# Performance work log

Measured on AMD Instinct MI355X. Metric: run time of the kernel, lower is better.

## Reference

```python
import jax, jax.numpy as jnp
import numpy as np

# Regularized layout for the per-batch masked attention:
#   batch_size B=8, each batch has NF=2048 'fill' points followed by NK=4096 'keep' points.
B, NF, NK = 8, 2048, 4096
C_IN, C_KQ, C_OUT = 256, 64, 256


def setup_inputs() -> dict:
    key = jax.random.key(0)
    ks = jax.random.split(key, 7)
    N = B * (NF + NK)
    features = jax.random.normal(ks[0], (N, C_IN), dtype=jnp.float32)
    # keep flag: 0 for fill points, 1 for keep points, per batch (fill-first layout)
    flag = jnp.tile(jnp.concatenate([jnp.zeros(NF, jnp.int32), jnp.ones(NK, jnp.int32)]), B)
    s = 1.0 / np.sqrt(C_IN)
    Wq = jax.random.normal(ks[1], (C_KQ, C_IN), jnp.float32) * s
    bq = jnp.zeros((C_KQ,), jnp.float32)
    Wk = jax.random.normal(ks[2], (C_KQ, C_IN), jnp.float32) * s
    bk = jnp.zeros((C_KQ,), jnp.float32)
    Wv = jax.random.normal(ks[3], (C_OUT, C_IN), jnp.float32) * s
    bv = jnp.zeros((C_OUT,), jnp.float32)
    return {"features": features, "keep_flag": flag,
            "Wq": Wq, "bq": bq, "Wk": Wk, "bk": bk, "Wv": Wv, "bv": bv}


def reference(features, keep_flag, Wq, bq, Wk, bk, Wv, bv):
    # features: [N, C_IN]; keep_flag encodes the fill/keep split, which in this
    # regular layout is: first NF rows of each batch are fill, remaining NK are keep.
    del keep_flag  # structure is encoded in the layout (fill-first per batch)
    f = features.reshape(B, NF + NK, C_IN)
    fill = f[:, :NF]             # [B, NF, C_IN]
    keep = f[:, NF:]             # [B, NK, C_IN]
    q = fill @ Wq.T + bq         # [B, NF, C_KQ]
    k = keep @ Wk.T + bk         # [B, NK, C_KQ]
    v = keep @ Wv.T + bv         # [B, NK, C_OUT]
    ratio = np.sqrt(C_KQ).astype(np.float32)
    scores = jnp.einsum('bfd,bkd->bfk', q, k) / ratio   # [B, NF, NK]
    attn = jax.nn.softmax(scores, axis=-1)
    out_fill = jnp.einsum('bfk,bkc->bfc', attn, v)      # [B, NF, C_OUT]
    # keep rows pass through unchanged (only fill rows are overwritten)
    out = jnp.concatenate([out_fill, keep], axis=1)
    return out.reshape(B * (NF + NK), C_OUT)
```

## Files before the change

kernel.cpp:

```cpp
#include <hip/hip_runtime.h>
#include <hip/hip_bf16.h>

#define BATCHES 8
#define NFILL 2048
#define NKEEP 4096
#define SEQLEN 6144
#define CIN 256
#define CKQ 64
#define COUT 256

#define KSC 0.18033688011112042f
#define KOFF -11.541560327111707f

typedef __bf16 bf16_t;
typedef float f32x4 __attribute__((ext_vector_type(4)));
typedef bf16_t bf16x8 __attribute__((ext_vector_type(8)));

__device__ inline void cvt8_store(bf16_t* dst, float4 a, float4 b) {
  bf16x8 v;
  v[0] = (bf16_t)a.x; v[1] = (bf16_t)a.y; v[2] = (bf16_t)a.z; v[3] = (bf16_t)a.w;
  v[4] = (bf16_t)b.x; v[5] = (bf16_t)b.y; v[6] = (bf16_t)b.z; v[7] = (bf16_t)b.w;
  *(bf16x8*)dst = v;
}

__global__ __launch_bounds__(256) void gemm_qk(
    const float* __restrict__ feat, const float* __restrict__ Wq,
    const float* __restrict__ bq, const float* __restrict__ Wk,
    const float* __restrict__ bk, bf16_t* __restrict__ Qw,
    bf16_t* __restrict__ Kw) {
  __shared__ bf16_t Xs[64][72];
  __shared__ bf16_t Ws[64][72];

  const int QBLOCKS = BATCHES * NFILL / 64;
  const bool isK = blockIdx.x >= QBLOCKS;
  const int mb = isK ? blockIdx.x - QBLOCKS : blockIdx.x;
  const float* W = isK ? Wk : Wq;
  const float* bias = isK ? bk : bq;
  bf16_t* outp = isK ? Kw : Qw;
  const int rpb_shift = isK ? 12 : 11;
  const int row_off = isK ? NFILL : 0;

  const int t = threadIdx.x;
  const int lane = t & 63;
  const int wv = t >> 6;
  const int l16 = lane & 15;
  const int quad = lane >> 4;

  const int lr = t >> 2;
  const int koff = (t & 3) << 4;
  const int mrow = mb * 64 + lr;
  const int batch = mrow >> rpb_shift;
  const int ridx = mrow & ((1 << rpb_shift) - 1);
  const float* xptr = feat + ((long)(batch * SEQLEN + row_off + ridx)) * CIN + koff;
  const float* wptr = W + ((long)lr) * CIN + koff;

  f32x4 acc[4];
#pragma unroll
  for (int nb = 0; nb < 4; nb++) acc[nb] = f32x4{0.f, 0.f, 0.f, 0.f};

  for (int k0 = 0; k0 < CIN; k0 += 64) {
    float4 x0 = *(const float4*)(xptr + k0);
    float4 x1 = *(const float4*)(xptr + k0 + 4);
    float4 x2 = *(const float4*)(xptr + k0 + 8);
    float4 x3 = *(const float4*)(xptr + k0 + 12);
    float4 w0 = *(const float4*)(wptr + k0);
    float4 w1 = *(const float4*)(wptr + k0 + 4);
    float4 w2 = *(const float4*)(wptr + k0 + 8);
    float4 w3 = *(const float4*)(wptr + k0 + 12);
    __syncthreads();
    cvt8_store(&Xs[lr][koff], x0, x1);
    cvt8_store(&Xs[lr][koff + 8], x2, x3);
    cvt8_store(&Ws[lr][koff], w0, w1);
    cvt8_store(&Ws[lr][koff + 8], w2, w3);
    __syncthreads();
#pragma unroll
    for (int ks = 0; ks < 2; ks++) {
      bf16x8 afrag = *(const bf16x8*)&Xs[wv * 16 + l16][ks * 32 + quad * 8];
#pragma unroll
      for (int nb = 0; nb < 4; nb++) {
        bf16x8 bfrag = *(const bf16x8*)&Ws[nb * 16 + l16][ks * 32 + quad * 8];
        acc[nb] = __builtin_amdgcn_mfma_f32_16x16x32_bf16(afrag, bfrag, acc[nb], 0, 0, 0);
      }
    }
  }

#pragma unroll
  for (int nb = 0; nb < 4; nb++) {
    const int n = nb * 16 + l16;
    const float bb = bias[n];
#pragma unroll
    for (int r = 0; r < 4; r++) {
      const int m = mb * 64 + wv * 16 + quad * 4 + r;
      outp[(long)m * CKQ + n] = (bf16_t)(acc[nb][r] + bb);
    }
  }
}

__global__ __launch_bounds__(256) void gemm_v(
    const float* __restrict__ feat, const float* __restrict__ Wv,
    const float* __restrict__ bv, bf16_t* __restrict__ Vw,
    float* __restrict__ outp) {
  __shared__ bf16_t Xs[64][264];
  __shared__ bf16_t Ws[64][72];
  __shared__ float Cs[64][68];

  const int mb = blockIdx.x;
  const int t = threadIdx.x;
  const int lane = t & 63;
  const int wv = t >> 6;
  const int l16 = lane & 15;
  const int quad = lane >> 4;

  const int lr = t >> 2;
  const int koff = (t & 3) << 4;

  const int grow = mb * 64 + lr;
  const int batch = grow >> 12;
  const int ridx = grow & 4095;
  const float* xptr = feat + ((long)(batch * SEQLEN + NFILL + ridx)) * CIN;
  float4* orow = (float4*)(outp + ((long)(batch * SEQLEN + NFILL + ridx)) * COUT);

#pragma unroll
  for (int j = 0; j < 4; j++) {
    const int c = koff + j * 64;
    float4 x0 = *(const float4*)(xptr + c);
    float4 x1 = *(const float4*)(xptr + c + 4);
    float4 x2 = *(const float4*)(xptr + c + 8);
    float4 x3 = *(const float4*)(xptr + c + 12);
    cvt8_store(&Xs[lr][c], x0, x1);
    cvt8_store(&Xs[lr][c + 8], x2, x3);
    orow[(c >> 2) + 0] = x0;
    orow[(c >> 2) + 1] = x1;
    orow[(c >> 2) + 2] = x2;
    orow[(c >> 2) + 3] = x3;
  }
  __syncthreads();

  const int vb = (mb * 64) >> 12;
  const int key0base = (mb * 64) & 4095;

  for (int nt = 0; nt < 4; nt++) {
    const int n0 = nt * 64;
    f32x4 acc[4];
#pragma unroll
    for (int nb = 0; nb < 4; nb++) acc[nb] = f32x4{0.f, 0.f, 0.f, 0.f};

    for (int k0 = 0; k0 < CIN; k0 += 64) {
      const float* wptr = Wv + ((long)(n0 + lr)) * CIN + k0 + koff;
      float4 w0 = *(const float4*)(wptr);
      float4 w1 = *(const float4*)(wptr + 4);
      float4 w2 = *(const float4*)(wptr + 8);
      float4 w3 = *(const float4*)(wptr + 12);
      __syncthreads();
      cvt8_store(&Ws[lr][koff], w0, w1);
      cvt8_store(&Ws[lr][koff + 8], w2, w3);
      __syncthreads();
#pragma unroll
      for (int ks = 0; ks < 2; ks++) {
        bf16x8 afrag = *(const bf16x8*)&Xs[wv * 16 + l16][k0 + ks * 32 + quad * 8];
#pragma unroll
        for (int nb = 0; nb < 4; nb++) {
          bf16x8 bfrag = *(const bf16x8*)&Ws[nb * 16 + l16][ks * 32 + quad * 8];
          acc[nb] = __builtin_amdgcn_mfma_f32_16x16x32_bf16(afrag, bfrag, acc[nb], 0, 0, 0);
        }
      }
    }

    __syncthreads();
#pragma unroll
    for (int nb = 0; nb < 4; nb++) {
      const float bb = bv[n0 + nb * 16 + l16];
#pragma unroll
      for (int r = 0; r < 4; r++)
        Cs[wv * 16 + quad * 4 + r][nb * 16 + l16] = acc[nb][r] + bb;
    }
    __syncthreads();
    const int c = t >> 2;
    const int seg = t & 3;
    bf16_t tmp[16];
#pragma unroll
    for (int i = 0; i < 16; i++) tmp[i] = (bf16_t)Cs[seg * 16 + i][c];
    bf16_t* dst = Vw + ((long)(vb * COUT + n0 + c)) * NKEEP + key0base + seg * 16;
    *(uint4*)dst = *(uint4*)tmp;
    *(uint4*)(dst + 8) = *(uint4*)(tmp + 8);
  }
}

__global__ __launch_bounds__(256) void attn_kernel(
    const bf16_t* __restrict__ Q, const bf16_t* __restrict__ K,
    const bf16_t* __restrict__ Vt, float* __restrict__ outp) {
  __shared__ bf16_t Ks[2][64][72];
  __shared__ bf16_t Ps[64][72];
  __shared__ float Lsh[64];

  const int qt = blockIdx.x;
  const int b = blockIdx.y;
  const int t = threadIdx.x;
  const int lane = t & 63;
  const int wv = t >> 6;
  const int l16 = lane & 15;
  const int quad = lane >> 4;

  const int krow = t >> 2;
  const int kcol = (t & 3) << 4;

  const bf16_t* kbase = K + (long)b * NKEEP * CKQ;
  const int c0 = wv * 64;
  const bf16_t* vlane =
      Vt + ((long)(b * COUT + c0 + l16)) * NKEEP + quad * 8;

  bf16x8 qfrag[2];
  {
    const bf16_t* qrow = Q + ((long)(b * NFILL + qt * 64 + wv * 16 + l16)) * CKQ;
#pragma unroll
    for (int ks = 0; ks < 2; ks++)
      qfrag[ks] = *(const bf16x8*)(qrow + ks * 32 + quad * 8);
  }

  f32x4 oacc[4][4];
#pragma unroll
  for (int m = 0; m < 4; m++)
#pragma unroll
    for (int ct = 0; ct < 4; ct++) oacc[m][ct] = f32x4{0.f, 0.f, 0.f, 0.f};
  float rsum[4] = {0.f, 0.f, 0.f, 0.f};

  uint4 kreg0, kreg1;
  bf16x8 vA[8], vB[8];

  {
    const bf16_t* ksrc = kbase + (long)krow * CKQ + kcol;
    uint4 k0 = *(const uint4*)ksrc;
    uint4 k1 = *(const uint4*)(ksrc + 8);
#pragma unroll
    for (int ct = 0; ct < 4; ct++)
#pragma unroll
      for (int ks = 0; ks < 2; ks++)
        vA[ct * 2 + ks] = *(const bf16x8*)(vlane + (long)ct * 16 * NKEEP + ks * 32);
    *(uint4*)&Ks[0][krow][kcol] = k0;
    *(uint4*)&Ks[0][krow][kcol + 8] = k1;
  }

#define ATTN_TILE(BUF, VCUR, VNEXT, TV)                                         \
  {                                                                             \
    __syncthreads(); \
    const int tn = ((TV) + 1 < 64) ? (TV) + 1 : 63;                             \
    {                                                                           \
      const bf16_t* ksrc = kbase + ((long)(tn * 64 + krow)) * CKQ + kcol;       \
      kreg0 = *(const uint4*)ksrc;                                              \
      kreg1 = *(const uint4*)(ksrc + 8);                                        \
      const bf16_t* vsrc = vlane + (long)tn * 64;                               \
      _Pragma("unroll") for (int ct = 0; ct < 4; ct++)                          \
          _Pragma("unroll") for (int ks = 0; ks < 2; ks++)                      \
              VNEXT[ct * 2 + ks] =                                              \
          *(const bf16x8*)(vsrc + (long)ct * 16 * NKEEP + ks * 32);             \
    }                                                                           \
    f32x4 sacc[4];                                                              \
    _Pragma("unroll") for (int nb = 0; nb < 4; nb++)                            \
        sacc[nb] = f32x4{0.f, 0.f, 0.f, 0.f};                                   \
    _Pragma("unroll") for (int ks = 0; ks < 2; ks++) {                          \
      _Pragma("unroll") for (int nb = 0; nb < 4; nb++) {                        \
        bf16x8 kfrag = *(const bf16x8*)&Ks[BUF][nb * 16 + l16][ks * 32 + quad * 8]; \
        sacc[nb] = __builtin_amdgcn_mfma_f32_16x16x32_bf16(qfrag[ks], kfrag,    \
                                                           sacc[nb], 0, 0, 0); \
      }                                                                         \
    }                                                                           \
    _Pragma("unroll") for (int nb = 0; nb < 4; nb++) {                          \
      _Pragma("unroll") for (int r = 0; r < 4; r++) {                           \
        const float p = __builtin_exp2f(fmaf(sacc[nb][r], KSC, KOFF));          \
        rsum[r] += p;                                                           \
        Ps[wv * 16 + quad * 4 + r][nb * 16 + l16] = (bf16_t)p;                  \
      }                                                                         \
    }                                                                           \
    asm volatile("s_waitcnt lgkmcnt(0)\n\ts_barrier" ::: "memory");      \
    _Pragma("unroll") for (int ks = 0; ks < 2; ks++) {                          \
      _Pragma("unroll") for (int m = 0; m < 4; m++) {                           \
        bf16x8 pfrag = *(const bf16x8*)&Ps[m * 16 + l16][ks * 32 + quad * 8];   \
        _Pragma("unroll") for (int ct = 0; ct < 4; ct++)                        \
            oacc[m][ct] = __builtin_amdgcn_mfma_f32_16x16x32_bf16(              \
                pfrag, VCUR[ct * 2 + ks], oacc[m][ct], 0, 0, 0);                \
      }                                                                         \
    }                                                                           \
    *(uint4*)&Ks[BUF ^ 1][krow][kcol] = kreg0;                                  \
    *(uint4*)&Ks[BUF ^ 1][krow][kcol + 8] = kreg1;                              \
  }

#pragma unroll 1
  for (int tv = 0; tv < 64; tv += 2) {
    ATTN_TILE(0, vA, vB, tv)
    ATTN_TILE(1, vB, vA, tv + 1)
  }
#undef ATTN_TILE

#pragma unroll
  for (int off = 1; off < 16; off <<= 1)
#pragma unroll
    for (int r = 0; r < 4; r++) rsum[r] += __shfl_xor(rsum[r], off, 64);
  if (l16 == 0) {
#pragma unroll
    for (int r = 0; r < 4; r++) Lsh[wv * 16 + quad * 4 + r] = rsum[r];
  }
  __syncthreads();

  float rl[4][4];
#pragma unroll
  for (int m = 0; m < 4; m++)
#pragma unroll
    for (int r = 0; r < 4; r++) rl[m][r] = 1.0f / Lsh[m * 16 + quad * 4 + r];

  const long obase = ((long)(b * SEQLEN + qt * 64)) * COUT + c0;
#pragma unroll
  for (int m = 0; m < 4; m++)
#pragma unroll
    for (int ct = 0; ct < 4; ct++)
#pragma unroll
      for (int r = 0; r < 4; r++)
        outp[obase + (long)(m * 16 + quad * 4 + r) * COUT + ct * 16 + l16] =
            oacc[m][ct][r] * rl[m][r];
}

extern "C" void kernel_launch(void* const* d_in, const int* in_sizes, int n_in,
                              void* d_out, int out_size, void* d_ws, size_t ws_size,
                              hipStream_t stream) {
  const float* feat = (const float*)d_in[0];
  const float* Wq = (const float*)d_in[2];
  const float* bq = (const float*)d_in[3];
  const float* Wk = (const float*)d_in[4];
  const float* bk = (const float*)d_in[5];
  const float* Wv = (const float*)d_in[6];
  const float* bv = (const float*)d_in[7];
  float* outp = (float*)d_out;

  bf16_t* Qw = (bf16_t*)d_ws;
  bf16_t* Kw = Qw + (size_t)BATCHES * NFILL * CKQ;
  bf16_t* Vw = Kw + (size_t)BATCHES * NKEEP * CKQ;

  gemm_qk<<<dim3(768), 256, 0, stream>>>(feat, Wq, bq, Wk, bk, Qw, Kw);
  gemm_v<<<dim3(512), 256, 0, stream>>>(feat, Wv, bv, Vw, outp);
  attn_kernel<<<dim3(NFILL / 64, BATCHES), 256, 0, stream>>>(Qw, Kw, Vw, outp);
}
```

Before: 216.0 us.

## Load K fragments directly to registers and double-buffer P in LDS

```diff
diff --git a/kernel.cpp b/kernel.cpp
--- a/kernel.cpp
+++ b/kernel.cpp
@@ -15,6 +15,7 @@
 typedef __bf16 bf16_t;
 typedef float f32x4 __attribute__((ext_vector_type(4)));
 typedef bf16_t bf16x8 __attribute__((ext_vector_type(8)));
+typedef bf16_t bf16x4 __attribute__((ext_vector_type(4)));
 
 __device__ inline void cvt8_store(bf16_t* dst, float4 a, float4 b) {
   bf16x8 v;
@@ -189,8 +190,7 @@
 __global__ __launch_bounds__(256) void attn_kernel(
     const bf16_t* __restrict__ Q, const bf16_t* __restrict__ K,
     const bf16_t* __restrict__ Vt, float* __restrict__ outp) {
-  __shared__ bf16_t Ks[2][64][72];
-  __shared__ bf16_t Ps[64][72];
+  __shared__ bf16_t Ps[2][64][72];
   __shared__ float Lsh[64];
 
   const int qt = blockIdx.x;
@@ -201,10 +201,8 @@
   const int l16 = lane & 15;
   const int quad = lane >> 4;
 
-  const int krow = t >> 2;
-  const int kcol = (t & 3) << 4;
-
-  const bf16_t* kbase = K + (long)b * NKEEP * CKQ;
+  const bf16_t* klane =
+      K + ((long)(b * NKEEP + l16)) * CKQ + quad * 8;
   const int c0 = wv * 64;
   const bf16_t* vlane =
       Vt + ((long)(b * COUT + c0 + l16)) * NKEEP + quad * 8;
@@ -222,83 +220,79 @@
   for (int m = 0; m < 4; m++)
 #pragma unroll
     for (int ct = 0; ct < 4; ct++) oacc[m][ct] = f32x4{0.f, 0.f, 0.f, 0.f};
-  float rsum[4] = {0.f, 0.f, 0.f, 0.f};
-
-  uint4 kreg0, kreg1;
-  bf16x8 vA[8], vB[8];
+  float rsum = 0.f;
+
+  bf16x8 kA[8], kB[8], vA[8], vB[8];
 
   {
-    const bf16_t* ksrc = kbase + (long)krow * CKQ + kcol;
-    uint4 k0 = *(const uint4*)ksrc;
-    uint4 k1 = *(const uint4*)(ksrc + 8);
+#pragma unroll
+    for (int kb = 0; kb < 4; kb++)
+#pragma unroll
+      for (int ks = 0; ks < 2; ks++)
+        kA[kb * 2 + ks] = *(const bf16x8*)(klane + (long)(kb * 16) * CKQ + ks * 32);
 #pragma unroll
     for (int ct = 0; ct < 4; ct++)
 #pragma unroll
       for (int ks = 0; ks < 2; ks++)
         vA[ct * 2 + ks] = *(const bf16x8*)(vlane + (long)ct * 16 * NKEEP + ks * 32);
-    *(uint4*)&Ks[0][krow][kcol] = k0;
-    *(uint4*)&Ks[0][krow][kcol + 8] = k1;
-  }
-
-#define ATTN_TILE(BUF, VCUR, VNEXT, TV)                                         \
+  }
+
+#define ATTN_TILE(PB, KCUR, KNXT, VCUR, VNXT, TV)                               \
   {                                                                             \
-    __syncthreads(); \
     const int tn = ((TV) + 1 < 64) ? (TV) + 1 : 63;                             \
     {                                                                           \
-      const bf16_t* ksrc = kbase + ((long)(tn * 64 + krow)) * CKQ + kcol;       \
-      kreg0 = *(const uint4*)ksrc;                                              \
-      kreg1 = *(const uint4*)(ksrc + 8);                                        \
+      const bf16_t* ksrc = klane + ((long)tn * 64) * CKQ;                       \
+      _Pragma("unroll") for (int kb = 0; kb < 4; kb++)                          \
+          _Pragma("unroll") for (int ks = 0; ks < 2; ks++)                      \
+              KNXT[kb * 2 + ks] =                                               \
+          *(const bf16x8*)(ksrc + (long)(kb * 16) * CKQ + ks * 32);             \
       const bf16_t* vsrc = vlane + (long)tn * 64;                               \
       _Pragma("unroll") for (int ct = 0; ct < 4; ct++)                          \
           _Pragma("unroll") for (int ks = 0; ks < 2; ks++)                      \
-              VNEXT[ct * 2 + ks] =                                              \
+              VNXT[ct * 2 + ks] =                                               \
           *(const bf16x8*)(vsrc + (long)ct * 16 * NKEEP + ks * 32);             \
     }                                                                           \
-    f32x4 sacc[4];                                                              \
-    _Pragma("unroll") for (int nb = 0; nb < 4; nb++)                            \
-        sacc[nb] = f32x4{0.f, 0.f, 0.f, 0.f};                                   \
+    f32x4 sacc[4];       \
+    _Pragma("unroll") for (int kb = 0; kb < 4; kb++)                            \
+        sacc[kb] = f32x4{0.f, 0.f, 0.f, 0.f};                                   \
     _Pragma("unroll") for (int ks = 0; ks < 2; ks++) {                          \
-      _Pragma("unroll") for (int nb = 0; nb < 4; nb++) {                        \
-        bf16x8 kfrag = *(const bf16x8*)&Ks[BUF][nb * 16 + l16][ks * 32 + quad * 8]; \
-        sacc[nb] = __builtin_amdgcn_mfma_f32_16x16x32_bf16(qfrag[ks], kfrag,    \
-                                                           sacc[nb], 0, 0, 0); \
+      _Pragma("unroll") for (int kb = 0; kb < 4; kb++) {                        \
+        sacc[kb] = __builtin_amdgcn_mfma_f32_16x16x32_bf16(                     \
+            KCUR[kb * 2 + ks], qfrag[ks], sacc[kb], 0, 0, 0);                   \
       }                                                                         \
     }                                                                           \
-    _Pragma("unroll") for (int nb = 0; nb < 4; nb++) {                          \
-      _Pragma("unroll") for (int r = 0; r < 4; r++) {                           \
-        const float p = __builtin_exp2f(fmaf(sacc[nb][r], KSC, KOFF));          \
-        rsum[r] += p;                                                           \
-        Ps[wv * 16 + quad * 4 + r][nb * 16 + l16] = (bf16_t)p;                  \
-      }                                                                         \
+    _Pragma("unroll") for (int kb = 0; kb < 4; kb++) {                          \
+      const float e0 = __builtin_exp2f(fmaf(sacc[kb][0], KSC, KOFF));           \
+      const float e1 = __builtin_exp2f(fmaf(sacc[kb][1], KSC, KOFF));           \
+      const float e2 = __builtin_exp2f(fmaf(sacc[kb][2], KSC, KOFF));           \
+      const float e3 = __builtin_exp2f(fmaf(sacc[kb][3], KSC, KOFF));           \
+      rsum += (e0 + e1) + (e2 + e3);                                            \
+      bf16x4 pk;                                                                \
+      pk[0] = (bf16_t)e0; pk[1] = (bf16_t)e1;                                   \
+      pk[2] = (bf16_t)e2; pk[3] = (bf16_t)e3;                                   \
+      *(bf16x4*)&Ps[PB][wv * 16 + l16][kb * 16 + quad * 4] = pk;                \
     }                                                                           \
-    asm volatile("s_waitcnt lgkmcnt(0)\n\ts_barrier" ::: "memory");      \
+    asm volatile("s_waitcnt lgkmcnt(0)\n\ts_barrier" ::: "memory");             \
     _Pragma("unroll") for (int ks = 0; ks < 2; ks++) {                          \
       _Pragma("unroll") for (int m = 0; m < 4; m++) {                           \
-        bf16x8 pfrag = *(const bf16x8*)&Ps[m * 16 + l16][ks * 32 + quad * 8];   \
+        bf16x8 pfrag = *(const bf16x8*)&Ps[PB][m * 16 + l16][ks * 32 + quad * 8]; \
         _Pragma("unroll") for (int ct = 0; ct < 4; ct++)                        \
             oacc[m][ct] = __builtin_amdgcn_mfma_f32_16x16x32_bf16(              \
                 pfrag, VCUR[ct * 2 + ks], oacc[m][ct], 0, 0, 0);                \
       }                                                                         \
     }                                                                           \
-    *(uint4*)&Ks[BUF ^ 1][krow][kcol] = kreg0;                                  \
-    *(uint4*)&Ks[BUF ^ 1][krow][kcol + 8] = kreg1;                              \
   }
 
 #pragma unroll 1
   for (int tv = 0; tv < 64; tv += 2) {
-    ATTN_TILE(0, vA, vB, tv)
-    ATTN_TILE(1, vB, vA, tv + 1)
+    ATTN_TILE(0, kA, kB, vA, vB, tv)
+    ATTN_TILE(1, kB, kA, vB, vA, tv + 1)
   }
 #undef ATTN_TILE
 
-#pragma unroll
-  for (int off = 1; off < 16; off <<= 1)
-#pragma unroll
-    for (int r = 0; r < 4; r++) rsum[r] += __shfl_xor(rsum[r], off, 64);
-  if (l16 == 0) {
-#pragma unroll
-    for (int r = 0; r < 4; r++) Lsh[wv * 16 + quad * 4 + r] = rsum[r];
-  }
+  rsum += __shfl_xor(rsum, 16, 64);
+  rsum += __shfl_xor(rsum, 32, 64);
+  if (quad == 0) Lsh[wv * 16 + l16] = rsum;
   __syncthreads();
 
   float rl[4][4];
```

New measurement: 258.4 us. +19.7%, slower.

## Fuse Q, K and V projections into one kernel sharing the staged keep tile

Applied to the files above, without the earlier changes.

```diff
diff --git a/kernel.cpp b/kernel.cpp
--- a/kernel.cpp
+++ b/kernel.cpp
@@ -23,22 +23,55 @@
   *(bf16x8*)dst = v;
 }
 
-__global__ __launch_bounds__(256) void gemm_qk(
+__device__ inline void proj_tile(const bf16_t (*Xs)[264], bf16_t (*Ws)[72],
+                                 const float* __restrict__ Wmat, int lr,
+                                 int koff, int wv, int l16, int quad,
+                                 f32x4 acc[4]) {
+  const float* wp = Wmat + (long)lr * CIN + koff;
+  float4 w0 = *(const float4*)(wp);
+  float4 w1 = *(const float4*)(wp + 4);
+  float4 w2 = *(const float4*)(wp + 8);
+  float4 w3 = *(const float4*)(wp + 12);
+#pragma unroll
+  for (int nb = 0; nb < 4; nb++) acc[nb] = f32x4{0.f, 0.f, 0.f, 0.f};
+#pragma unroll
+  for (int k0 = 0; k0 < CIN; k0 += 64) {
+    const int kn = (k0 + 64 < CIN) ? k0 + 64 : k0;
+    float4 n0 = *(const float4*)(wp + kn);
+    float4 n1 = *(const float4*)(wp + kn + 4);
+    float4 n2 = *(const float4*)(wp + kn + 8);
+    float4 n3 = *(const float4*)(wp + kn + 12);
+    __syncthreads();
+    cvt8_store(&Ws[lr][koff], w0, w1);
+    cvt8_store(&Ws[lr][koff + 8], w2, w3);
+    __syncthreads();
+#pragma unroll
+    for (int ks = 0; ks < 2; ks++) {
+      bf16x8 afrag = *(const bf16x8*)&Xs[wv * 16 + l16][k0 + ks * 32 + quad * 8];
+#pragma unroll
+      for (int nb = 0; nb < 4; nb++) {
+        bf16x8 bfrag = *(const bf16x8*)&Ws[nb * 16 + l16][ks * 32 + quad * 8];
+        acc[nb] = __builtin_amdgcn_mfma_f32_16x16x32_bf16(afrag, bfrag, acc[nb], 0, 0, 0);
+      }
+    }
+    w0 = n0; w1 = n1; w2 = n2; w3 = n3;
+  }
+}
+
+__global__ __launch_bounds__(256) void gemm_qkv(
     const float* __restrict__ feat, const float* __restrict__ Wq,
     const float* __restrict__ bq, const float* __restrict__ Wk,
-    const float* __restrict__ bk, bf16_t* __restrict__ Qw,
-    bf16_t* __restrict__ Kw) {
-  __shared__ bf16_t Xs[64][72];
+    const float* __restrict__ bk, const float* __restrict__ Wv,
+    const float* __restrict__ bv, bf16_t* __restrict__ Qw,
+    bf16_t* __restrict__ Kw, bf16_t* __restrict__ Vw,
+    float* __restrict__ outp) {
+  __shared__ bf16_t Xs[64][264];
   __shared__ bf16_t Ws[64][72];
-
-  const int QBLOCKS = BATCHES * NFILL / 64;
-  const bool isK = blockIdx.x >= QBLOCKS;
-  const int mb = isK ? blockIdx.x - QBLOCKS : blockIdx.x;
-  const float* W = isK ? Wk : Wq;
-  const float* bias = isK ? bk : bq;
-  bf16_t* outp = isK ? Kw : Qw;
-  const int rpb_shift = isK ? 12 : 11;
-  const int row_off = isK ? NFILL : 0;
+  __shared__ float Cs[64][68];
+
+  const int bid = blockIdx.x;
+  const bool isQ = bid >= 512;
+  const int mb = isQ ? bid - 512 : bid;
 
   const int t = threadIdx.x;
   const int lane = t & 63;
@@ -48,77 +81,15 @@
 
   const int lr = t >> 2;
   const int koff = (t & 3) << 4;
+
   const int mrow = mb * 64 + lr;
+  const int rpb_shift = isQ ? 11 : 12;
   const int batch = mrow >> rpb_shift;
   const int ridx = mrow & ((1 << rpb_shift) - 1);
-  const float* xptr = feat + ((long)(batch * SEQLEN + row_off + ridx)) * CIN + koff;
-  const float* wptr = W + ((long)lr) * CIN + koff;
-
-  f32x4 acc[4];
-#pragma unroll
-  for (int nb = 0; nb < 4; nb++) acc[nb] = f32x4{0.f, 0.f, 0.f, 0.f};
-
-  for (int k0 = 0; k0 < CIN; k0 += 64) {
-    float4 x0 = *(const float4*)(xptr + k0);
-    float4 x1 = *(const float4*)(xptr + k0 + 4);
-    float4 x2 = *(const float4*)(xptr + k0 + 8);
-    float4 x3 = *(const float4*)(xptr + k0 + 12);
-    float4 w0 = *(const float4*)(wptr + k0);
-    float4 w1 = *(const float4*)(wptr + k0 + 4);
-    float4 w2 = *(const float4*)(wptr + k0 + 8);
-    float4 w3 = *(const float4*)(wptr + k0 + 12);
-    __syncthreads();
-    cvt8_store(&Xs[lr][koff], x0, x1);
-    cvt8_store(&Xs[lr][koff + 8], x2, x3);
-    cvt8_store(&Ws[lr][koff], w0, w1);
-    cvt8_store(&Ws[lr][koff + 8], w2, w3);
-    __syncthreads();
-#pragma unroll
-    for (int ks = 0; ks < 2; ks++) {
-      bf16x8 afrag = *(const bf16x8*)&Xs[wv * 16 + l16][ks * 32 + quad * 8];
-#pragma unroll
-      for (int nb = 0; nb < 4; nb++) {
-        bf16x8 bfrag = *(const bf16x8*)&Ws[nb * 16 + l16][ks * 32 + quad * 8];
-        acc[nb] = __builtin_amdgcn_mfma_f32_16x16x32_bf16(afrag, bfrag, acc[nb], 0, 0, 0);
-      }
-    }
-  }
-
-#pragma unroll
-  for (int nb = 0; nb < 4; nb++) {
-    const int n = nb * 16 + l16;
-    const float bb = bias[n];
-#pragma unroll
-    for (int r = 0; r < 4; r++) {
-      const int m = mb * 64 + wv * 16 + quad * 4 + r;
-      outp[(long)m * CKQ + n] = (bf16_t)(acc[nb][r] + bb);
-    }
-  }
-}
-
-__global__ __launch_bounds__(256) void gemm_v(
-    const float* __restrict__ feat, const float* __restrict__ Wv,
-    const float* __restrict__ bv, bf16_t* __restrict__ Vw,
-    float* __restrict__ outp) {
-  __shared__ bf16_t Xs[64][264];
-  __shared__ bf16_t Ws[64][72];
-  __shared__ float Cs[64][68];
-
-  const int mb = blockIdx.x;
-  const int t = threadIdx.x;
-  const int lane = t & 63;
-  const int wv = t >> 6;
-  const int l16 = lane & 15;
-  const int quad = lane >> 4;
-
-  const int lr = t >> 2;
-  const int koff = (t & 3) << 4;
-
-  const int grow = mb * 64 + lr;
-  const int batch = grow >> 12;
-  const int ridx = grow & 4095;
-  const float* xptr = feat + ((long)(batch * SEQLEN + NFILL + ridx)) * CIN;
-  float4* orow = (float4*)(outp + ((long)(batch * SEQLEN + NFILL + ridx)) * COUT);
+  const int row_off = isQ ? 0 : NFILL;
+  const long grow = (long)(batch * SEQLEN + row_off + ridx);
+  const float* xptr = feat + grow * CIN;
+  float4* orow = (float4*)(outp + grow * COUT);
 
 #pragma unroll
   for (int j = 0; j < 4; j++) {
@@ -129,42 +100,49 @@
     float4 x3 = *(const float4*)(xptr + c + 12);
     cvt8_store(&Xs[lr][c], x0, x1);
     cvt8_store(&Xs[lr][c + 8], x2, x3);
-    orow[(c >> 2) + 0] = x0;
-    orow[(c >> 2) + 1] = x1;
-    orow[(c >> 2) + 2] = x2;
-    orow[(c >> 2) + 3] = x3;
+    if (!isQ) {
+      orow[(c >> 2) + 0] = x0;
+      orow[(c >> 2) + 1] = x1;
+      orow[(c >> 2) + 2] = x2;
+      orow[(c >> 2) + 3] = x3;
+    }
   }
   __syncthreads();
+
+  f32x4 acc[4];
+
+  if (isQ) {
+    proj_tile(Xs, Ws, Wq, lr, koff, wv, l16, quad, acc);
+#pragma unroll
+    for (int nb = 0; nb < 4; nb++) {
+      const int n = nb * 16 + l16;
+      const float bb = bq[n];
+#pragma unroll
+      for (int r = 0; r < 4; r++) {
+        const int m = mb * 64 + wv * 16 + quad * 4 + r;
+        Qw[(long)m * CKQ + n] = (bf16_t)(acc[nb][r] + bb);
+      }
+    }
+    return;
+  }
+
+  proj_tile(Xs, Ws, Wk, lr, koff, wv, l16, quad, acc);
+#pragma unroll
+  for (int nb = 0; nb < 4; nb++) {
+    const int n = nb * 16 + l16;
+    const float bb = bk[n];
+#pragma unroll
+    for (int r = 0; r < 4; r++) {
+      const int m = mb * 64 + wv * 16 + quad * 4 + r;
+      Kw[(long)m * CKQ + n] = (bf16_t)(acc[nb][r] + bb);
+    }
+  }
 
   const int vb = (mb * 64) >> 12;
   const int key0base = (mb * 64) & 4095;
-
   for (int nt = 0; nt < 4; nt++) {
     const int n0 = nt * 64;
-    f32x4 acc[4];
-#pragma unroll
-    for (int nb = 0; nb < 4; nb++) acc[nb] = f32x4{0.f, 0.f, 0.f, 0.f};
-
-    for (int k0 = 0; k0 < CIN; k0 += 64) {
-      const float* wptr = Wv + ((long)(n0 + lr)) * CIN + k0 + koff;
-      float4 w0 = *(const float4*)(wptr);
-      float4 w1 = *(const float4*)(wptr + 4);
-      float4 w2 = *(const float4*)(wptr + 8);
-      float4 w3 = *(const float4*)(wptr + 12);
-      __syncthreads();
-      cvt8_store(&Ws[lr][koff], w0, w1);
-      cvt8_store(&Ws[lr][koff + 8], w2, w3);
-      __syncthreads();
-#pragma unroll
-      for (int ks = 0; ks < 2; ks++) {
-        bf16x8 afrag = *(const bf16x8*)&Xs[wv * 16 + l16][k0 + ks * 32 + quad * 8];
-#pragma unroll
-        for (int nb = 0; nb < 4; nb++) {
-          bf16x8 bfrag = *(const bf16x8*)&Ws[nb * 16 + l16][ks * 32 + quad * 8];
-          acc[nb] = __builtin_amdgcn_mfma_f32_16x16x32_bf16(afrag, bfrag, acc[nb], 0, 0, 0);
-        }
-      }
-    }
+    proj_tile(Xs, Ws, Wv + (long)n0 * CIN, lr, koff, wv, l16, quad, acc);
 
     __syncthreads();
 #pragma unroll
@@ -334,7 +312,7 @@
   bf16_t* Kw = Qw + (size_t)BATCHES * NFILL * CKQ;
   bf16_t* Vw = Kw + (size_t)BATCHES * NKEEP * CKQ;
 
-  gemm_qk<<<dim3(768), 256, 0, stream>>>(feat, Wq, bq, Wk, bk, Qw, Kw);
-  gemm_v<<<dim3(512), 256, 0, stream>>>(feat, Wv, bv, Vw, outp);
+  gemm_qkv<<<dim3(768), 256, 0, stream>>>(feat, Wq, bq, Wk, bk, Wv, bv,
+                                          Qw, Kw, Vw, outp);
   attn_kernel<<<dim3(NFILL / 64, BATCHES), 256, 0, stream>>>(Qw, Kw, Vw, outp);
 }
```

After: 207.1 us. 1.04x faster.
